# Kernel optimization log

Measured on AMD Instinct MI355X. Metric: run time of the kernel, lower is better.

Reference implementation:

```python
import jax, jax.numpy as jnp
import numpy as np

NUM_EXPERTS = 8
TOP_K = 2
N_EMBD = 1024
D_FFN = 2048  # 4*N_EMBD // TOP_K, already multiple of BLOCK_N=128
BLOCK_M = 128
NORM_TOPK = True


def setup_inputs() -> dict:
    key = jax.random.key(0)
    k1, k2, k3 = jax.random.split(key, 3)
    x = jax.random.normal(k1, (2, 2048, N_EMBD), dtype=jnp.float32)
    router_w = jax.random.normal(k2, (NUM_EXPERTS, N_EMBD), dtype=jnp.float32) * 0.02
    w1 = jax.random.normal(k3, (N_EMBD, D_FFN * NUM_EXPERTS), dtype=jnp.float32) * 0.02
    return {"x": x, "router_w": router_w, "w1": w1}


def reference(x, router_w, w1):
    B, S, H = x.shape
    x_flat = x.reshape(-1, H)                                   # [T, H]
    router_logits = x_flat @ router_w.T                         # [T, E]
    probs = jax.nn.softmax(router_logits.astype(jnp.float32), axis=-1)
    rweights, sel = jax.lax.top_k(probs, TOP_K)                 # [T, k]
    if NORM_TOPK:
        rweights = rweights / rweights.sum(axis=-1, keepdims=True)
    rweights = rweights.astype(x.dtype)

    # repeat_interleave tokens top_k times, then stable-sort by expert id
    x_rep = jnp.repeat(x_flat, TOP_K, axis=0)                   # [M, H]
    sel_rep = sel.reshape(-1)                                   # [M]
    rw_rep = rweights.reshape(-1, 1)                            # [M, 1]
    order = jnp.argsort(sel_rep, stable=True)                   # expert-sort permutation
    x_grouped = x_rep[order]                                    # [M, H]
    sel_sorted = sel_rep[order]                                 # [M]
    rw_sorted = rw_rep[order]                                   # [M, 1]

    M = x_grouped.shape[0]
    nblk = M // BLOCK_M                                         # M divisible by BLOCK_M by construction
    # SDD kernel: expert of the first row of each BLOCK_M block selects w1 slice
    block_expert = sel_sorted[::BLOCK_M]                        # [nblk] == col_indices_ptr
    w1e = w1.reshape(H, NUM_EXPERTS, D_FFN)                     # w1[:, e*D:(e+1)*D] == w1e[:, e, :]
    w_blk = jnp.take(w1e, block_expert, axis=1)                 # [H, nblk, D]
    x_blk = x_grouped.reshape(nblk, BLOCK_M, H)                 # [nblk, Bm, H]
    block_sparse = jnp.einsum('bmh,hbd->bmd', x_blk, w_blk).reshape(M, D_FFN)

    block_sparse = jax.nn.gelu(block_sparse, approximate=False) * rw_sorted
    return block_sparse, router_logits
```

## Files before the change

### kernel.cpp

```cpp
#include <hip/hip_runtime.h>
#include <hip/hip_bf16.h>
#include <cmath>

typedef float f32x16 __attribute__((ext_vector_type(16)));
typedef __bf16 bf16x8 __attribute__((ext_vector_type(8)));
typedef __bf16 bf16x4 __attribute__((ext_vector_type(4)));

#define NE 8
#define H 1024
#define DF 2048
#define WCOLS 16384
#define NTOK 4096
#define MROWS 8192
#define NBLK 64


typedef const __attribute__((address_space(1))) unsigned int glb_u32;
typedef __attribute__((address_space(3))) unsigned int lds_u32;

__device__ __forceinline__ void async_load16(const void* g, void* l) {
    __builtin_amdgcn_global_load_lds((glb_u32*)g, (lds_u32*)l, 16, 0, 0);
}

__global__ __launch_bounds__(256) void prep_kernel(
    const float* __restrict__ x, const float* __restrict__ rw,
    const float* __restrict__ w1,
    float* __restrict__ logits, int* __restrict__ sel, float* __restrict__ rwn,
    __bf16* __restrict__ xb, __bf16* __restrict__ Wt)
{
    __shared__ float tile[32][132];
    int b = blockIdx.x;
    int tid = threadIdx.x;
    if (b < 1024) {
        int tok  = b * 4 + (tid >> 6);
        int lane = tid & 63;
        const float* xr = x + (size_t)tok * H;
        __bf16* xbr = xb + (size_t)tok * H;
        float acc[NE];
#pragma unroll
        for (int e = 0; e < NE; ++e) acc[e] = 0.f;
#pragma unroll
        for (int it = 0; it < 4; ++it) {
            int k = (it * 64 + lane) * 4;
            float4 xv = *(const float4*)(xr + k);
            bf16x4 xc;
            xc[0] = (__bf16)xv.x; xc[1] = (__bf16)xv.y;
            xc[2] = (__bf16)xv.z; xc[3] = (__bf16)xv.w;
            *(bf16x4*)(xbr + k) = xc;
#pragma unroll
            for (int e = 0; e < NE; ++e) {
                float4 wv = *(const float4*)(rw + e * H + k);
                acc[e] += xv.x * wv.x + xv.y * wv.y + xv.z * wv.z + xv.w * wv.w;
            }
        }
#pragma unroll
        for (int e = 0; e < NE; ++e) {
            float v = acc[e];
#pragma unroll
            for (int off = 32; off > 0; off >>= 1) v += __shfl_xor(v, off, 64);
            acc[e] = v;
        }
        if (lane == 0) {
#pragma unroll
            for (int e = 0; e < NE; ++e) logits[tok * NE + e] = acc[e];
            int i1 = 0; float m1 = acc[0];
#pragma unroll
            for (int e = 1; e < NE; ++e) if (acc[e] > m1) { m1 = acc[e]; i1 = e; }
            int i2 = -1; float m2 = -INFINITY;
#pragma unroll
            for (int e = 0; e < NE; ++e) if (e != i1 && acc[e] > m2) { m2 = acc[e]; i2 = e; }
            float e2 = expf(m2 - m1);
            float inv = 1.f / (1.f + e2);
            sel[tok * 2]     = i1;  sel[tok * 2 + 1] = i2;
            rwn[tok * 2]     = inv; rwn[tok * 2 + 1] = e2 * inv;
        }
        return;
    }
    int g  = b - 1024;
    int c  = g >> 5;
    int kb = g & 31;
    int kk = tid >> 3;
    int cc = (tid & 7) * 16;
    const float* src = w1 + (size_t)(kb * 32 + kk) * WCOLS + c * 128 + cc;
#pragma unroll
    for (int i = 0; i < 4; ++i) {
        float4 v = *(const float4*)(src + i * 4);
        *(float4*)&tile[kk][cc + i * 4] = v;
    }
    __syncthreads();
    int n = tid >> 1, kc0 = (tid & 1) * 16;
    bf16x8 o0, o1;
#pragma unroll
    for (int i = 0; i < 8; ++i) {
        o0[i] = (__bf16)tile[kc0 + i][n];
        o1[i] = (__bf16)tile[kc0 + 8 + i][n];
    }
    size_t tile_id = (size_t)(c >> 1) * 32 + kb;
    int group  = (c & 1) * 4 + (n >> 5);
    int chunk0 = kc0 >> 3;
    __bf16* dst = Wt + tile_id * 8192 + group * 1024 + chunk0 * 256 + (n & 31) * 8;
    *(bf16x8*)dst         = o0;
    *(bf16x8*)(dst + 256) = o1;
}

__global__ __launch_bounds__(1024) void sort_kernel(
    const int* __restrict__ sel, const float* __restrict__ rwn,
    int* __restrict__ stok, float* __restrict__ srw, int* __restrict__ bexp)
{
    __shared__ int cnt[NE][1024];
    __shared__ int wtot[NE][2];
    __shared__ int ebase[NE + 1];
    int t = threadIdx.x;
    int selv[8];
    int lc[NE];
#pragma unroll
    for (int e = 0; e < NE; ++e) lc[e] = 0;
    int base = t * 8;
#pragma unroll
    for (int j = 0; j < 8; ++j) { selv[j] = sel[base + j]; lc[selv[j]]++; }
#pragma unroll
    for (int e = 0; e < NE; ++e) cnt[e][t] = lc[e];
    __syncthreads();
    int g = t >> 7, j = t & 127, jl = j & 63;
    int s = 0, pre[8];
#pragma unroll
    for (int i = 0; i < 8; ++i) { pre[i] = s; s += cnt[g][j * 8 + i]; }
    int inc = s;
#pragma unroll
    for (int d = 1; d < 64; d <<= 1) {
        int v = __shfl_up(inc, d, 64);
        if (jl >= d) inc += v;
    }
    if (jl == 63) wtot[g][j >> 6] = inc;
    __syncthreads();
    int add = (j >= 64) ? wtot[g][0] : 0;
    int excl = inc - s + add;
#pragma unroll
    for (int i = 0; i < 8; ++i) cnt[g][j * 8 + i] = excl + pre[i];
    __syncthreads();
    if (t == 0) {
        int acc = 0;
        for (int e = 0; e < NE; ++e) { ebase[e] = acc; acc += wtot[e][0] + wtot[e][1]; }
        ebase[NE] = acc;
    }
    __syncthreads();
    int off[NE];
#pragma unroll
    for (int e = 0; e < NE; ++e) off[e] = ebase[e] + cnt[e][t];
#pragma unroll
    for (int j2 = 0; j2 < 8; ++j2) {
        int i = base + j2;
        int e = selv[j2];
        int pos = off[e]++;
        stok[pos] = i >> 1;
        srw[pos]  = rwn[i];
    }
    __syncthreads();
    if (t < NBLK) {
        int r = t * 128;
        int e = 0;
        while (e < NE - 1 && r >= ebase[e + 1]) ++e;
        bexp[t] = e;
    }
}

__global__ __launch_bounds__(256, 2) void moe_gemm(
    const __bf16* __restrict__ xb, const __bf16* __restrict__ Wt,
    const int* __restrict__ stok, const float* __restrict__ srw,
    const int* __restrict__ bexp, float* __restrict__ out)
{
    __shared__ __align__(16) __bf16 smem[3 * 12288];
    __shared__ int   tokS[128];
    __shared__ float rwS[128];

    int g = blockIdx.x;
    int by  = (g & 7) * 8 + ((g >> 3) & 7);
    int bxp = g >> 6;
    int tid = threadIdx.x;
    if (tid < 128) {
        tokS[tid] = stok[by * 128 + tid];
        rwS[tid]  = srw[by * 128 + tid];
    }
    int e = bexp[by];
    __syncthreads();

    int lane = tid & 63;
    int wv   = tid >> 6;
    int l32  = lane & 31;
    int hi   = lane >> 5;

    const __bf16* aSrc = xb + (size_t)tokS[wv * 32 + l32] * H + hi * 8;
    const __bf16* bSrc = Wt + (size_t)(e * 8 + bxp) * 32 * 8192 + wv * 2048 + lane * 8;
    __bf16* aDst = smem + wv * 1024 + lane * 8;
    __bf16* bDst = smem + 4096 + wv * 2048 + lane * 8;

#define STAGE(kt, bb) do {                                                     \
        const __bf16* aN = aSrc + (kt) * 32;                                   \
        const __bf16* bN = bSrc + (size_t)(kt) * 8192;                         \
        __bf16* aD = aDst + (bb) * 12288;                                      \
        __bf16* bD = bDst + (bb) * 12288;                                      \
        async_load16(aN,        aD);                                           \
        async_load16(aN + 16,   aD + 512);                                     \
        async_load16(bN,        bD);                                           \
        async_load16(bN + 512,  bD + 512);                                     \
        async_load16(bN + 1024, bD + 1024);                                    \
        async_load16(bN + 1536, bD + 1536);                                    \
    } while (0)

    int wm = (wv & 1) * 64;
    int wn = (wv >> 1) * 128;
    int ag = (wv & 1) * 2;
    int bg = (wv >> 1) * 4;

    f32x16 acc[2][4];
#pragma unroll
    for (int i = 0; i < 2; ++i)
#pragma unroll
        for (int j = 0; j < 4; ++j)
#pragma unroll
            for (int r = 0; r < 16; ++r) acc[i][j][r] = 0.f;

    STAGE(0, 0);
    STAGE(1, 1);

    int cur = 0, nxt = 2;
    for (int kb = 0; kb < 32; ++kb) {
        if (kb < 31) asm volatile("s_waitcnt vmcnt(6)" ::: "memory");
        else         asm volatile("s_waitcnt vmcnt(0)" ::: "memory");
        __builtin_amdgcn_s_barrier();
        __builtin_amdgcn_sched_barrier(0);
        if (kb < 30) STAGE(kb + 2, nxt);

        const __bf16* Ab = smem + cur * 12288;
        const __bf16* Bb = Ab + 4096;
        bf16x8 af[2][2], bfr[4][2];
#pragma unroll
        for (int h = 0; h < 2; ++h) {
#pragma unroll
            for (int ti = 0; ti < 2; ++ti)
                af[ti][h] = *(const bf16x8*)&Ab[(ag + ti) * 1024 + (h * 2 + hi) * 256 + l32 * 8];
#pragma unroll
            for (int tj = 0; tj < 4; ++tj)
                bfr[tj][h] = *(const bf16x8*)&Bb[(bg + tj) * 1024 + (h * 2 + hi) * 256 + l32 * 8];
        }
        __builtin_amdgcn_s_setprio(1);
#pragma unroll
        for (int h = 0; h < 2; ++h)
#pragma unroll
            for (int ti = 0; ti < 2; ++ti)
#pragma unroll
                for (int tj = 0; tj < 4; ++tj)
                    acc[ti][tj] = __builtin_amdgcn_mfma_f32_32x32x16_bf16(
                        af[ti][h], bfr[tj][h], acc[ti][tj], 0, 0, 0);
        __builtin_amdgcn_s_setprio(0);

        cur = (cur == 2) ? 0 : cur + 1;
        nxt = (nxt == 2) ? 0 : nxt + 1;
    }
#undef STAGE

    int rowh = hi * 4;
#pragma unroll
    for (int ti = 0; ti < 2; ++ti)
#pragma unroll
        for (int reg = 0; reg < 16; ++reg) {
            int row = (reg & 3) + 8 * (reg >> 2) + rowh;
            int m = wm + ti * 32 + row;
            float rw = rwS[m];
            size_t ob = (size_t)(by * 128 + m) * DF + bxp * 256 + wn + l32;
#pragma unroll
            for (int tj = 0; tj < 4; ++tj) {
                float val = acc[ti][tj][reg];
                float u = 0.7978845608028654f * val * (1.f + 0.044715f * val * val);
                float t = __expf(-2.f * fabsf(u));
                float th = (1.f - t) / (1.f + t);
                th = u < 0.f ? -th : th;
                out[ob + tj * 32] = 0.5f * val * (1.f + th) * rw;
            }
        }
}

extern "C" void kernel_launch(void* const* d_in, const int* in_sizes, int n_in,
                              void* d_out, int out_size, void* d_ws, size_t ws_size,
                              hipStream_t stream) {
    (void)in_sizes; (void)n_in; (void)out_size; (void)ws_size;
    const float* x        = (const float*)d_in[0];
    const float* router_w = (const float*)d_in[1];
    const float* w1       = (const float*)d_in[2];
    float* out    = (float*)d_out;
    float* logits = out + (size_t)MROWS * DF;

    char* ws    = (char*)d_ws;
    int*   sel  = (int*)(ws);
    float* rwn  = (float*)(ws + 0x8000);
    int*   stok = (int*)(ws + 0x10000);
    float* srw  = (float*)(ws + 0x18000);
    int*   bexp = (int*)(ws + 0x20000);
    __bf16* xb  = (__bf16*)(ws + (1 << 20));
    __bf16* Wt  = (__bf16*)(ws + (1 << 20) + (8 << 20));

    prep_kernel<<<5120, 256, 0, stream>>>(x, router_w, w1, logits, sel, rwn, xb, Wt);
    sort_kernel<<<1, 1024, 0, stream>>>(sel, rwn, stok, srw, bexp);
    moe_gemm<<<512, 256, 0, stream>>>(xb, Wt, stok, srw, bexp, out);
}
```

Baseline: 191.2 us.

## Restructure pipeline: separate router, fuse weight transpose with sort, shrink GEMM tiles

Splits the old prep kernel into a router kernel and a mid kernel. The mid kernel does the w1 fp32-to-bf16 transpose with per-thread strided column reads and runs the expert sort in one extra block of 256 threads, instead of a separate single-block launch. The GEMM tile drops from 128x256 with K-step 32 to 128x128 with K-step 16, with smaller LDS stages and occupancy hint 4, doubling the grid to 1024 blocks. This trades fewer loads per MFMA and more K iterations for higher occupancy. The strided uncoalesced w1 reads may be costly.

New measurement: 200.8 us. 5.0% more time.

```diff
diff --git a/kernel.cpp b/kernel.cpp
--- a/kernel.cpp
+++ b/kernel.cpp
@@ -22,125 +22,117 @@
     __builtin_amdgcn_global_load_lds((glb_u32*)g, (lds_u32*)l, 16, 0, 0);
 }
 
-__global__ __launch_bounds__(256) void prep_kernel(
+__global__ __launch_bounds__(256) void router_kernel(
     const float* __restrict__ x, const float* __restrict__ rw,
-    const float* __restrict__ w1,
     float* __restrict__ logits, int* __restrict__ sel, float* __restrict__ rwn,
-    __bf16* __restrict__ xb, __bf16* __restrict__ Wt)
+    __bf16* __restrict__ xb)
 {
-    __shared__ float tile[32][132];
     int b = blockIdx.x;
     int tid = threadIdx.x;
-    if (b < 1024) {
-        int tok  = b * 4 + (tid >> 6);
-        int lane = tid & 63;
-        const float* xr = x + (size_t)tok * H;
-        __bf16* xbr = xb + (size_t)tok * H;
-        float acc[NE];
-#pragma unroll
-        for (int e = 0; e < NE; ++e) acc[e] = 0.f;
-#pragma unroll
-        for (int it = 0; it < 4; ++it) {
-            int k = (it * 64 + lane) * 4;
-            float4 xv = *(const float4*)(xr + k);
-            bf16x4 xc;
-            xc[0] = (__bf16)xv.x; xc[1] = (__bf16)xv.y;
-            xc[2] = (__bf16)xv.z; xc[3] = (__bf16)xv.w;
-            *(bf16x4*)(xbr + k) = xc;
-#pragma unroll
-            for (int e = 0; e < NE; ++e) {
-                float4 wv = *(const float4*)(rw + e * H + k);
-                acc[e] += xv.x * wv.x + xv.y * wv.y + xv.z * wv.z + xv.w * wv.w;
-            }
+    int tok  = b * 4 + (tid >> 6);
+    int lane = tid & 63;
+    const float* xr = x + (size_t)tok * H;
+    __bf16* xbr = xb + (size_t)tok * H;
+    float acc[NE];
+#pragma unroll
+    for (int e = 0; e < NE; ++e) acc[e] = 0.f;
+#pragma unroll
+    for (int it = 0; it < 4; ++it) {
+        int k = (it * 64 + lane) * 4;
+        float4 xv = *(const float4*)(xr + k);
+        bf16x4 xc;
+        xc[0] = (__bf16)xv.x; xc[1] = (__bf16)xv.y;
+        xc[2] = (__bf16)xv.z; xc[3] = (__bf16)xv.w;
+        *(bf16x4*)(xbr + k) = xc;
+#pragma unroll
+        for (int e = 0; e < NE; ++e) {
+            float4 wv = *(const float4*)(rw + e * H + k);
+            acc[e] += xv.x * wv.x + xv.y * wv.y + xv.z * wv.z + xv.w * wv.w;
         }
-#pragma unroll
-        for (int e = 0; e < NE; ++e) {
-            float v = acc[e];
-#pragma unroll
-            for (int off = 32; off > 0; off >>= 1) v += __shfl_xor(v, off, 64);
-            acc[e] = v;
-        }
-        if (lane == 0) {
-#pragma unroll
-            for (int e = 0; e < NE; ++e) logits[tok * NE + e] = acc[e];
-            int i1 = 0; float m1 = acc[0];
-#pragma unroll
-            for (int e = 1; e < NE; ++e) if (acc[e] > m1) { m1 = acc[e]; i1 = e; }
-            int i2 = -1; float m2 = -INFINITY;
-#pragma unroll
-            for (int e = 0; e < NE; ++e) if (e != i1 && acc[e] > m2) { m2 = acc[e]; i2 = e; }
-            float e2 = expf(m2 - m1);
-            float inv = 1.f / (1.f + e2);
-            sel[tok * 2]     = i1;  sel[tok * 2 + 1] = i2;
-            rwn[tok * 2]     = inv; rwn[tok * 2 + 1] = e2 * inv;
-        }
-        return;
-    }
-    int g  = b - 1024;
-    int c  = g >> 5;
-    int kb = g & 31;
-    int kk = tid >> 3;
-    int cc = (tid & 7) * 16;
-    const float* src = w1 + (size_t)(kb * 32 + kk) * WCOLS + c * 128 + cc;
-#pragma unroll
-    for (int i = 0; i < 4; ++i) {
-        float4 v = *(const float4*)(src + i * 4);
-        *(float4*)&tile[kk][cc + i * 4] = v;
-    }
-    __syncthreads();
-    int n = tid >> 1, kc0 = (tid & 1) * 16;
-    bf16x8 o0, o1;
-#pragma unroll
-    for (int i = 0; i < 8; ++i) {
-        o0[i] = (__bf16)tile[kc0 + i][n];
-        o1[i] = (__bf16)tile[kc0 + 8 + i][n];
-    }
-    size_t tile_id = (size_t)(c >> 1) * 32 + kb;
-    int group  = (c & 1) * 4 + (n >> 5);
-    int chunk0 = kc0 >> 3;
-    __bf16* dst = Wt + tile_id * 8192 + group * 1024 + chunk0 * 256 + (n & 31) * 8;
-    *(bf16x8*)dst         = o0;
-    *(bf16x8*)(dst + 256) = o1;
-}
-
-__global__ __launch_bounds__(1024) void sort_kernel(
+    }
+#pragma unroll
+    for (int e = 0; e < NE; ++e) {
+        float v = acc[e];
+#pragma unroll
+        for (int off = 32; off > 0; off >>= 1) v += __shfl_xor(v, off, 64);
+        acc[e] = v;
+    }
+    if (lane == 0) {
+#pragma unroll
+        for (int e = 0; e < NE; ++e) logits[tok * NE + e] = acc[e];
+        int i1 = 0; float m1 = acc[0];
+#pragma unroll
+        for (int e = 1; e < NE; ++e) if (acc[e] > m1) { m1 = acc[e]; i1 = e; }
+        int i2 = -1; float m2 = -INFINITY;
+#pragma unroll
+        for (int e = 0; e < NE; ++e) if (e != i1 && acc[e] > m2) { m2 = acc[e]; i2 = e; }
+        float e2 = expf(m2 - m1);
+        float inv = 1.f / (1.f + e2);
+        sel[tok * 2]     = i1;  sel[tok * 2 + 1] = i2;
+        rwn[tok * 2]     = inv; rwn[tok * 2 + 1] = e2 * inv;
+    }
+}
+
+__global__ __launch_bounds__(256) void mid_kernel(
+    const float* __restrict__ w1, __bf16* __restrict__ Wt,
     const int* __restrict__ sel, const float* __restrict__ rwn,
     int* __restrict__ stok, float* __restrict__ srw, int* __restrict__ bexp)
 {
-    __shared__ int cnt[NE][1024];
-    __shared__ int wtot[NE][2];
+    __shared__ int cnt[NE][256];
+    __shared__ int wtot[NE];
     __shared__ int ebase[NE + 1];
+    int b = blockIdx.x;
     int t = threadIdx.x;
-    int selv[8];
+
+    if (b < 8192) {
+        int q = b * 256 + t;
+        int row   = q & 31;
+        int chunk = (q >> 5) & 3;
+        int grp   = (q >> 7) & 7;
+        int kb    = (q >> 10) & 31;
+        int ep    = q >> 15;
+        int col   = ep * 256 + grp * 32 + row;
+        int k0    = kb * 32 + chunk * 8;
+        const float* src = w1 + (size_t)k0 * WCOLS + col;
+        bf16x8 o;
+#pragma unroll
+        for (int j = 0; j < 8; ++j) o[j] = (__bf16)src[(size_t)j * WCOLS];
+        *(bf16x8*)(Wt + (size_t)q * 8) = o;
+        return;
+    }
+
+    int selv[32];
     int lc[NE];
 #pragma unroll
     for (int e = 0; e < NE; ++e) lc[e] = 0;
-    int base = t * 8;
-#pragma unroll
-    for (int j = 0; j < 8; ++j) { selv[j] = sel[base + j]; lc[selv[j]]++; }
+    int base = t * 32;
+#pragma unroll
+    for (int j = 0; j < 32; ++j) { selv[j] = sel[base + j]; lc[selv[j]]++; }
 #pragma unroll
     for (int e = 0; e < NE; ++e) cnt[e][t] = lc[e];
     __syncthreads();
-    int g = t >> 7, j = t & 127, jl = j & 63;
-    int s = 0, pre[8];
-#pragma unroll
-    for (int i = 0; i < 8; ++i) { pre[i] = s; s += cnt[g][j * 8 + i]; }
-    int inc = s;
-#pragma unroll
-    for (int d = 1; d < 64; d <<= 1) {
-        int v = __shfl_up(inc, d, 64);
-        if (jl >= d) inc += v;
-    }
-    if (jl == 63) wtot[g][j >> 6] = inc;
-    __syncthreads();
-    int add = (j >= 64) ? wtot[g][0] : 0;
-    int excl = inc - s + add;
-#pragma unroll
-    for (int i = 0; i < 8; ++i) cnt[g][j * 8 + i] = excl + pre[i];
+    int l = t & 63;
+#pragma unroll
+    for (int ee = 0; ee < 2; ++ee) {
+        int e = (t >> 6) * 2 + ee;
+        int s = 0, pre[4];
+#pragma unroll
+        for (int i = 0; i < 4; ++i) { pre[i] = s; s += cnt[e][l * 4 + i]; }
+        int inc = s;
+#pragma unroll
+        for (int d = 1; d < 64; d <<= 1) {
+            int v = __shfl_up(inc, d, 64);
+            if (l >= d) inc += v;
+        }
+        if (l == 63) wtot[e] = inc;
+        int excl = inc - s;
+#pragma unroll
+        for (int i = 0; i < 4; ++i) cnt[e][l * 4 + i] = excl + pre[i];
+    }
     __syncthreads();
     if (t == 0) {
         int acc = 0;
-        for (int e = 0; e < NE; ++e) { ebase[e] = acc; acc += wtot[e][0] + wtot[e][1]; }
+        for (int e = 0; e < NE; ++e) { ebase[e] = acc; acc += wtot[e]; }
         ebase[NE] = acc;
     }
     __syncthreads();
@@ -148,9 +140,9 @@
 #pragma unroll
     for (int e = 0; e < NE; ++e) off[e] = ebase[e] + cnt[e][t];
 #pragma unroll
-    for (int j2 = 0; j2 < 8; ++j2) {
-        int i = base + j2;
-        int e = selv[j2];
+    for (int j = 0; j < 32; ++j) {
+        int i = base + j;
+        int e = selv[j];
         int pos = off[e]++;
         stok[pos] = i >> 1;
         srw[pos]  = rwn[i];
@@ -164,18 +156,18 @@
     }
 }
 
-__global__ __launch_bounds__(256, 2) void moe_gemm(
+__global__ __launch_bounds__(256, 4) void moe_gemm(
     const __bf16* __restrict__ xb, const __bf16* __restrict__ Wt,
     const int* __restrict__ stok, const float* __restrict__ srw,
     const int* __restrict__ bexp, float* __restrict__ out)
 {
-    __shared__ __align__(16) __bf16 smem[3 * 12288];
+    __shared__ __align__(16) __bf16 smem[3 * 4096];
     __shared__ int   tokS[128];
     __shared__ float rwS[128];
 
     int g = blockIdx.x;
-    int by  = (g & 7) * 8 + ((g >> 3) & 7);
-    int bxp = g >> 6;
+    int by = (g & 7) * 8 + ((g >> 3) & 7);
+    int bx = g >> 6;
     int tid = threadIdx.x;
     if (tid < 128) {
         tokS[tid] = stok[by * 128 + tid];
@@ -189,73 +181,65 @@
     int l32  = lane & 31;
     int hi   = lane >> 5;
 
-    const __bf16* aSrc = xb + (size_t)tokS[wv * 32 + l32] * H + hi * 8;
-    const __bf16* bSrc = Wt + (size_t)(e * 8 + bxp) * 32 * 8192 + wv * 2048 + lane * 8;
-    __bf16* aDst = smem + wv * 1024 + lane * 8;
-    __bf16* bDst = smem + 4096 + wv * 2048 + lane * 8;
-
-#define STAGE(kt, bb) do {                                                     \
-        const __bf16* aN = aSrc + (kt) * 32;                                   \
-        const __bf16* bN = bSrc + (size_t)(kt) * 8192;                         \
-        __bf16* aD = aDst + (bb) * 12288;                                      \
-        __bf16* bD = bDst + (bb) * 12288;                                      \
-        async_load16(aN,        aD);                                           \
-        async_load16(aN + 16,   aD + 512);                                     \
-        async_load16(bN,        bD);                                           \
-        async_load16(bN + 512,  bD + 512);                                     \
-        async_load16(bN + 1024, bD + 1024);                                    \
-        async_load16(bN + 1536, bD + 1536);                                    \
+    const __bf16* aSrcT = xb + (size_t)tokS[(tid >> 6) * 32 + (tid & 31)] * H
+                             + ((tid >> 5) & 1) * 8;
+    const __bf16* bSrcT = Wt + (size_t)(e * 8 + (bx >> 1)) * 262144
+                             + ((bx & 1) * 4 + (tid >> 6)) * 1024
+                             + ((tid * 8) & 511);
+    __bf16* aDst = smem + tid * 8;
+    __bf16* bDst = smem + 2048 + tid * 8;
+
+#define STAGE(kt_, bb_) do {                                                   \
+        int koff_ = (((kt_) >> 1) << 13) + (((kt_) & 1) << 9);                 \
+        async_load16(aSrcT + (kt_) * 16, aDst + (bb_) * 4096);                 \
+        async_load16(bSrcT + koff_,      bDst + (bb_) * 4096);                 \
     } while (0)
 
     int wm = (wv & 1) * 64;
-    int wn = (wv >> 1) * 128;
-    int ag = (wv & 1) * 2;
-    int bg = (wv >> 1) * 4;
-
-    f32x16 acc[2][4];
+    int wn = (wv >> 1) * 64;
+    int agb = (wv & 1) * 2;
+    int bgb = (wv >> 1) * 2;
+    int rdo = hi * 256 + l32 * 8;
+
+    f32x16 acc[2][2];
 #pragma unroll
     for (int i = 0; i < 2; ++i)
 #pragma unroll
-        for (int j = 0; j < 4; ++j)
+        for (int j = 0; j < 2; ++j)
 #pragma unroll
             for (int r = 0; r < 16; ++r) acc[i][j][r] = 0.f;
 
     STAGE(0, 0);
     STAGE(1, 1);
 
-    int cur = 0, nxt = 2;
-    for (int kb = 0; kb < 32; ++kb) {
-        if (kb < 31) asm volatile("s_waitcnt vmcnt(6)" ::: "memory");
+    int cur = 0;
+    for (int kt = 0; kt < 64; ++kt) {
+        if (kt < 63) asm volatile("s_waitcnt vmcnt(2)" ::: "memory");
         else         asm volatile("s_waitcnt vmcnt(0)" ::: "memory");
         __builtin_amdgcn_s_barrier();
         __builtin_amdgcn_sched_barrier(0);
-        if (kb < 30) STAGE(kb + 2, nxt);
-
-        const __bf16* Ab = smem + cur * 12288;
-        const __bf16* Bb = Ab + 4096;
-        bf16x8 af[2][2], bfr[4][2];
-#pragma unroll
-        for (int h = 0; h < 2; ++h) {
-#pragma unroll
-            for (int ti = 0; ti < 2; ++ti)
-                af[ti][h] = *(const bf16x8*)&Ab[(ag + ti) * 1024 + (h * 2 + hi) * 256 + l32 * 8];
-#pragma unroll
-            for (int tj = 0; tj < 4; ++tj)
-                bfr[tj][h] = *(const bf16x8*)&Bb[(bg + tj) * 1024 + (h * 2 + hi) * 256 + l32 * 8];
-        }
+        int nb = cur + 2; if (nb >= 3) nb -= 3;
+        if (kt < 62) STAGE(kt + 2, nb);
+
+        const __bf16* Ab = smem + cur * 4096;
+        bf16x8 af[2], bfr[2];
+#pragma unroll
+        for (int ti = 0; ti < 2; ++ti)
+            af[ti]  = *(const bf16x8*)&Ab[(agb + ti) * 512 + rdo];
+#pragma unroll
+        for (int tj = 0; tj < 2; ++tj)
+            bfr[tj] = *(const bf16x8*)&Ab[2048 + (bgb + tj) * 512 + rdo];
+
         __builtin_amdgcn_s_setprio(1);
 #pragma unroll
-        for (int h = 0; h < 2; ++h)
-#pragma unroll
-            for (int ti = 0; ti < 2; ++ti)
-#pragma unroll
-                for (int tj = 0; tj < 4; ++tj)
-                    acc[ti][tj] = __builtin_amdgcn_mfma_f32_32x32x16_bf16(
-                        af[ti][h], bfr[tj][h], acc[ti][tj], 0, 0, 0);
+        for (int ti = 0; ti < 2; ++ti)
+#pragma unroll
+            for (int tj = 0; tj < 2; ++tj)
+                acc[ti][tj] = __builtin_amdgcn_mfma_f32_32x32x16_bf16(
+                    af[ti], bfr[tj], acc[ti][tj], 0, 0, 0);
         __builtin_amdgcn_s_setprio(0);
 
-        cur = (cur == 2) ? 0 : cur + 1;
-        nxt = (nxt == 2) ? 0 : nxt + 1;
+        cur = cur + 1; if (cur >= 3) cur -= 3;
     }
 #undef STAGE
 
@@ -267,9 +251,9 @@
             int row = (reg & 3) + 8 * (reg >> 2) + rowh;
             int m = wm + ti * 32 + row;
             float rw = rwS[m];
-            size_t ob = (size_t)(by * 128 + m) * DF + bxp * 256 + wn + l32;
-#pragma unroll
-            for (int tj = 0; tj < 4; ++tj) {
+            size_t ob = (size_t)(by * 128 + m) * DF + bx * 128 + wn + l32;
+#pragma unroll
+            for (int tj = 0; tj < 2; ++tj) {
                 float val = acc[ti][tj][reg];
                 float u = 0.7978845608028654f * val * (1.f + 0.044715f * val * val);
                 float t = __expf(-2.f * fabsf(u));
@@ -299,7 +283,7 @@
     __bf16* xb  = (__bf16*)(ws + (1 << 20));
     __bf16* Wt  = (__bf16*)(ws + (1 << 20) + (8 << 20));
 
-    prep_kernel<<<5120, 256, 0, stream>>>(x, router_w, w1, logits, sel, rwn, xb, Wt);
-    sort_kernel<<<1, 1024, 0, stream>>>(sel, rwn, stok, srw, bexp);
-    moe_gemm<<<512, 256, 0, stream>>>(xb, Wt, stok, srw, bexp, out);
-}
+    router_kernel<<<1024, 256, 0, stream>>>(x, router_w, logits, sel, rwn, xb);
+    mid_kernel<<<8193, 256, 0, stream>>>(w1, Wt, sel, rwn, stok, srw, bexp);
+    moe_gemm<<<1024, 256, 0, stream>>>(xb, Wt, stok, srw, bexp, out);
+}
```
